# Optimization experiments

Hardware: AMD Instinct MI355X
Metric: run time of the kernel (lower is better)

Reference implementation:

```python
import jax, jax.numpy as jnp
import numpy as np

N = 50000
E = 800000
EPS = 1e-16
NEG_SLOPE = 0.2

def setup_inputs() -> dict:
    key = jax.random.key(0)
    ks = jax.random.split(key, 10)
    s = lambda fan: 1.0 / np.sqrt(fan)
    return {
        "x": jax.random.normal(ks[0], (N, 128), dtype=jnp.float32),
        "edge_index": jax.random.randint(ks[1], (2, E), 0, N, dtype=jnp.int64),
        "W1": jax.random.normal(ks[2], (128, 4 * 32), dtype=jnp.float32) * s(128),
        "att_src1": jax.random.normal(ks[3], (4, 32), dtype=jnp.float32) * s(32),
        "att_dst1": jax.random.normal(ks[4], (4, 32), dtype=jnp.float32) * s(32),
        "b1": jnp.zeros((128,), dtype=jnp.float32),
        "W2": jax.random.normal(ks[5], (128, 2), dtype=jnp.float32) * s(128),
        "att_src2": jax.random.normal(ks[6], (1, 2), dtype=jnp.float32) * s(2),
        "att_dst2": jax.random.normal(ks[7], (1, 2), dtype=jnp.float32) * s(2),
        "b2": jnp.zeros((2,), dtype=jnp.float32),
    }

def _gat_conv(x, src, dst, W, att_src, att_dst, bias, heads, out_ch, concat):
    n = x.shape[0]
    h = (x @ W).reshape(n, heads, out_ch)                      # [N,H,C]
    a_src = jnp.sum(h * att_src[None], axis=-1)                # [N,H]
    a_dst = jnp.sum(h * att_dst[None], axis=-1)                # [N,H]
    e = jax.nn.leaky_relu(a_src[src] + a_dst[dst], NEG_SLOPE)  # [Etot,H]
    # segment softmax over incoming edges per destination node
    m = jax.ops.segment_max(e, dst, num_segments=n)            # [N,H]
    m = jnp.where(jnp.isfinite(m), m, 0.0)
    ex = jnp.exp(e - m[dst])
    denom = jax.ops.segment_sum(ex, dst, num_segments=n)       # [N,H]
    alpha = ex / (denom[dst] + EPS)                            # [Etot,H]
    out = jax.ops.segment_sum(alpha[:, :, None] * h[src], dst, num_segments=n)  # [N,H,C]
    if concat:
        out = out.reshape(n, heads * out_ch)
    else:
        out = out.mean(axis=1)
    return out + bias

def reference(x, edge_index, W1, att_src1, att_dst1, b1, W2, att_src2, att_dst2, b2):
    n = x.shape[0]
    # PyG GATConv adds self-loops by default
    loops = jnp.arange(n, dtype=edge_index.dtype)
    src = jnp.concatenate([edge_index[0], loops])
    dst = jnp.concatenate([edge_index[1], loops])
    # dropout is identity at inference
    h = jax.nn.elu(_gat_conv(x, src, dst, W1, att_src1, att_dst1, b1, 4, 32, True))
    h = _gat_conv(h, src, dst, W2, att_src2, att_dst2, b2, 1, 2, False)
    return jax.nn.log_softmax(h, axis=1)
```

## Files before the change

kernel.cpp:

```cpp
#include <hip/hip_runtime.h>
#include <hip/hip_bf16.h>

#define NN 50000
#define EE 800000
#define CAP 64
#define CSTRIDE 16
#define NEG_SLOPE 0.2f
#define EPSF 1e-16f
#define BUILD_BLOCKS 4096
#define GEMM_BLOCKS ((NN + 63) / 64)
#define NPAIRS (EE / 2)
#define WROW 136
#define PROBE_IDX (NN * CSTRIDE)

typedef unsigned int uint32;
typedef __attribute__((ext_vector_type(8))) short short8;
typedef __attribute__((ext_vector_type(4))) float floatx4;

__device__ __forceinline__ unsigned short f2bf(float f) {
  unsigned int u = __float_as_uint(f);
  unsigned int r = (u + 0x7fffu + ((u >> 16) & 1u)) >> 16;
  return (unsigned short)r;
}
__device__ __forceinline__ float bf_lo(uint32 v) { return __uint_as_float(v << 16); }
__device__ __forceinline__ float bf_hi(uint32 v) { return __uint_as_float(v & 0xffff0000u); }
__device__ __forceinline__ float lrelu(float e) { return fmaxf(e, NEG_SLOPE * e); }

__device__ __forceinline__ void do_build(int b, const int* __restrict__ ei,
                                         int* __restrict__ counts,
                                         int* __restrict__ csr, uint32 P) {
  const int range = b & 7;
  const int lo = range * (NN / 8);
  const int hi = lo + (NN / 8);
  const int group = b >> 3;
  const int tid0 = group * 256 + threadIdx.x;
  const int stride = (BUILD_BLOCKS >> 3) * 256;

  { int n = lo + tid0; if (n < hi) csr[n * CAP] = n; }

  const int2* __restrict__ dst2 = (const int2*)(ei + EE);
  const int2* __restrict__ src2 = (const int2*)(ei);
  for (int p = tid0; p < NPAIRS; p += stride) {
    int2 d2 = dst2[p];
    int2 s2 = src2[p];
    if (d2.x >= lo && d2.x < hi) {
      uint32 k = (uint32)atomicAdd(&counts[d2.x * CSTRIDE], 1) - P;
      if (k < CAP - 1) csr[d2.x * CAP + k + 1] = s2.x;
    }
    if (d2.y >= lo && d2.y < hi) {
      uint32 k = (uint32)atomicAdd(&counts[d2.y * CSTRIDE], 1) - P;
      if (k < CAP - 1) csr[d2.y * CAP + k + 1] = s2.y;
    }
  }
}

__device__ __forceinline__ void do_gemm_tile(
    int tile, const float* __restrict__ x, const unsigned short* __restrict__ WtL,
    const float* __restrict__ att_src1, const float* __restrict__ att_dst1,
    uint32* __restrict__ h1b, float* __restrict__ as1, float* __restrict__ ad1) {
  const int t    = threadIdx.x;
  const int wave = t >> 6;
  const int lane = t & 63;
  const int quad = lane >> 4;
  const int col  = lane & 15;
  const int nodeBase = tile * 64 + wave * 16;

  floatx4 acc[8];
  #pragma unroll
  for (int i = 0; i < 8; i++) acc[i] = (floatx4){0.f, 0.f, 0.f, 0.f};

  int mread = nodeBase + col; if (mread >= NN) mread = NN - 1;
  const float* __restrict__ xrow = x + (size_t)mread * 128 + quad * 8;
  const unsigned short* __restrict__ bbase = WtL + col * WROW + quad * 8;

  #pragma unroll
  for (int ks = 0; ks < 4; ks++) {
    float4 a0 = *(const float4*)(xrow + ks * 32);
    float4 a1 = *(const float4*)(xrow + ks * 32 + 4);
    union { short8 v; unsigned short u[8]; } af;
    af.u[0] = f2bf(a0.x); af.u[1] = f2bf(a0.y);
    af.u[2] = f2bf(a0.z); af.u[3] = f2bf(a0.w);
    af.u[4] = f2bf(a1.x); af.u[5] = f2bf(a1.y);
    af.u[6] = f2bf(a1.z); af.u[7] = f2bf(a1.w);
    #pragma unroll
    for (int tt = 0; tt < 8; tt++) {
      short8 bf = *(const short8*)(bbase + tt * 16 * WROW + ks * 32);
      acc[tt] = __builtin_amdgcn_mfma_f32_16x16x32_bf16(af.v, bf, acc[tt], 0, 0, 0);
    }
  }

  float asv[8], adv[8];
  #pragma unroll
  for (int tt = 0; tt < 8; tt++) {
    asv[tt] = att_src1[tt * 16 + col];
    adv[tt] = att_dst1[tt * 16 + col];
  }

  #pragma unroll
  for (int r = 0; r < 4; r++) {
    const int gn = nodeBase + quad * 4 + r;
    const bool live = (gn < NN);
    #pragma unroll
    for (int tt = 0; tt < 8; tt++) {
      float v = acc[tt][r];
      float w = __shfl_xor(v, 1, 64);
      if (live && ((col & 1) == 0)) {
        uint32 pk = (uint32)f2bf(v) | ((uint32)f2bf(w) << 16);
        h1b[(size_t)gn * 64 + tt * 8 + (col >> 1)] = pk;
      }
    }
    #pragma unroll
    for (int h = 0; h < 4; h++) {
      float ps = acc[2 * h][r] * asv[2 * h] + acc[2 * h + 1][r] * asv[2 * h + 1];
      float pd = acc[2 * h][r] * adv[2 * h] + acc[2 * h + 1][r] * adv[2 * h + 1];
      #pragma unroll
      for (int off = 1; off < 16; off <<= 1) {
        ps += __shfl_xor(ps, off, 64);
        pd += __shfl_xor(pd, off, 64);
      }
      if (live && col == 0) {
        as1[gn * 4 + h] = ps;
        ad1[gn * 4 + h] = pd;
      }
    }
  }
}

__global__ __launch_bounds__(256) void work_k(
    const int* __restrict__ ei, int* __restrict__ counts, int* __restrict__ csr,
    const float* __restrict__ x, const float* __restrict__ W1,
    const float* __restrict__ att_src1, const float* __restrict__ att_dst1,
    uint32* __restrict__ h1b, float* __restrict__ as1, float* __restrict__ ad1) {
  __shared__ unsigned short WtL[128 * WROW];
  const int b = blockIdx.x;
  if (b < GEMM_BLOCKS) {
    const int c  = threadIdx.x & 127;
    const int kh = (threadIdx.x >> 7) * 4;
    #pragma unroll
    for (int k0 = kh; k0 < 128; k0 += 8) {
      unsigned short w0 = f2bf(W1[(k0 + 0) * 128 + c]);
      unsigned short w1 = f2bf(W1[(k0 + 1) * 128 + c]);
      unsigned short w2 = f2bf(W1[(k0 + 2) * 128 + c]);
      unsigned short w3 = f2bf(W1[(k0 + 3) * 128 + c]);
      uint32 lo = (uint32)w0 | ((uint32)w1 << 16);
      uint32 hi = (uint32)w2 | ((uint32)w3 << 16);
      *(uint2*)&WtL[c * WROW + k0] = make_uint2(lo, hi);
    }
    __syncthreads();
    do_gemm_tile(b, x, WtL, att_src1, att_dst1, h1b, as1, ad1);
  } else {
    const uint32 P =
        (uint32)__builtin_amdgcn_readfirstlane(counts[PROBE_IDX]);
    do_build(b - GEMM_BLOCKS, ei, counts, csr, P);
  }
}

__global__ __launch_bounds__(256) void agg1_k(
    const int* __restrict__ counts, const int* __restrict__ csr,
    const uint32* __restrict__ h1b, const float* __restrict__ as1,
    const float* __restrict__ ad1, const float* __restrict__ b1,
    const float* __restrict__ W2, const float* __restrict__ att_src2,
    const float* __restrict__ att_dst2, float4* __restrict__ rec) {
  const int lane = threadIdx.x & 63;
  const int wv = threadIdx.x >> 6;
  const int hd = lane >> 4;
  const int n = __builtin_amdgcn_readfirstlane(blockIdx.x * 4 + wv);

  const uint32 P = (uint32)__builtin_amdgcn_readfirstlane(counts[PROBE_IDX]);
  int cnt = (int)((uint32)counts[n * CSTRIDE] - P) + 1;
  cnt = __builtin_amdgcn_readfirstlane(cnt < CAP ? cnt : CAP);
  const int* __restrict__ row = csr + n * CAP;
  const float adv = ad1[n * 4 + hd];

  float den = 0.f, accx = 0.f, accy = 0.f;
  int j = 0;
  for (; j + 3 < cnt; j += 4) {
    int s0 = __builtin_amdgcn_readfirstlane(row[j]);
    int s1 = __builtin_amdgcn_readfirstlane(row[j + 1]);
    int s2 = __builtin_amdgcn_readfirstlane(row[j + 2]);
    int s3 = __builtin_amdgcn_readfirstlane(row[j + 3]);
    float e0 = as1[s0 * 4 + hd] + adv;
    float e1 = as1[s1 * 4 + hd] + adv;
    float e2 = as1[s2 * 4 + hd] + adv;
    float e3 = as1[s3 * 4 + hd] + adv;
    uint32 v0 = h1b[s0 * 64 + lane];
    uint32 v1 = h1b[s1 * 64 + lane];
    uint32 v2 = h1b[s2 * 64 + lane];
    uint32 v3 = h1b[s3 * 64 + lane];
    e0 = lrelu(e0); e1 = lrelu(e1); e2 = lrelu(e2); e3 = lrelu(e3);
    float x0 = __expf(e0), x1 = __expf(e1), x2 = __expf(e2), x3 = __expf(e3);
    den += (x0 + x1) + (x2 + x3);
    accx = fmaf(x0, bf_lo(v0), accx);
    accy = fmaf(x0, bf_hi(v0), accy);
    accx = fmaf(x1, bf_lo(v1), accx);
    accy = fmaf(x1, bf_hi(v1), accy);
    accx = fmaf(x2, bf_lo(v2), accx);
    accy = fmaf(x2, bf_hi(v2), accy);
    accx = fmaf(x3, bf_lo(v3), accx);
    accy = fmaf(x3, bf_hi(v3), accy);
  }
  for (; j < cnt; j++) {
    int s = __builtin_amdgcn_readfirstlane(row[j]);
    float e = lrelu(as1[s * 4 + hd] + adv);
    float ex = __expf(e);
    uint32 v = h1b[s * 64 + lane];
    den += ex;
    accx = fmaf(ex, bf_lo(v), accx);
    accy = fmaf(ex, bf_hi(v), accy);
  }

  float inv = 1.f / (den + EPSF);
  float2 bb = ((const float2*)b1)[lane];
  float ox = accx * inv + bb.x;
  float oy = accy * inv + bb.y;
  ox = (ox > 0.f) ? ox : (__expf(ox) - 1.f);
  oy = (oy > 0.f) ? oy : (__expf(oy) - 1.f);

  float4 wq = ((const float4*)W2)[lane];
  float p0 = ox * wq.x + oy * wq.z;
  float p1 = ox * wq.y + oy * wq.w;
  #pragma unroll
  for (int off = 32; off; off >>= 1) {
    p0 += __shfl_xor(p0, off, 64);
    p1 += __shfl_xor(p1, off, 64);
  }
  if (lane == 0) {
    rec[n] = make_float4(p0, p1,
                         p0 * att_src2[0] + p1 * att_src2[1],
                         p0 * att_dst2[0] + p1 * att_dst2[1]);
  }
}

__global__ __launch_bounds__(256) void agg2_k(
    const int* __restrict__ counts, const int* __restrict__ csr,
    const float4* __restrict__ rec, const float* __restrict__ b2,
    float* __restrict__ out) {
  int i = blockIdx.x * 256 + threadIdx.x;
  if (i >= NN * 8) return;
  int n = i >> 3;
  int sub = i & 7;
  const float adv = rec[n].w;
  const uint32 P = (uint32)__builtin_amdgcn_readfirstlane(counts[PROBE_IDX]);
  int cnt = (int)((uint32)counts[n * CSTRIDE] - P) + 1;
  cnt = cnt < CAP ? cnt : CAP;
  const int* __restrict__ row = csr + n * CAP;

  float den = 0.f, a0 = 0.f, a1 = 0.f;
  for (int j = sub; j < cnt; j += 8) {
    int s = row[j];
    float4 rs = rec[s];
    float e = lrelu(rs.z + adv);
    float ex = __expf(e);
    den += ex;
    a0 = fmaf(ex, rs.x, a0);
    a1 = fmaf(ex, rs.y, a1);
  }
  #pragma unroll
  for (int off = 4; off; off >>= 1) {
    den += __shfl_down(den, off, 8);
    a0  += __shfl_down(a0, off, 8);
    a1  += __shfl_down(a1, off, 8);
  }
  if (sub == 0) {
    float inv = 1.f / (den + EPSF);
    float o0 = a0 * inv + b2[0];
    float o1 = a1 * inv + b2[1];
    float mx = fmaxf(o0, o1);
    float lse = mx + __logf(__expf(o0 - mx) + __expf(o1 - mx));
    *(float2*)&out[n * 2] = make_float2(o0 - lse, o1 - lse);
  }
}

extern "C" void kernel_launch(void* const* d_in, const int* in_sizes, int n_in,
                              void* d_out, int out_size, void* d_ws, size_t ws_size,
                              hipStream_t stream) {
  const float* x        = (const float*)d_in[0];
  const int*   ei       = (const int*)d_in[1];
  const float* W1       = (const float*)d_in[2];
  const float* att_src1 = (const float*)d_in[3];
  const float* att_dst1 = (const float*)d_in[4];
  const float* b1       = (const float*)d_in[5];
  const float* W2       = (const float*)d_in[6];
  const float* att_src2 = (const float*)d_in[7];
  const float* att_dst2 = (const float*)d_in[8];
  const float* b2       = (const float*)d_in[9];
  float* out = (float*)d_out;

  char* p = (char*)d_ws;
  auto alloc = [&](size_t bytes) {
    char* r = p;
    p += (bytes + 255) & ~size_t(255);
    return r;
  };
  uint32* h1b  = (uint32*)alloc(sizeof(uint32) * NN * 64);
  float* as1   = (float*)alloc(sizeof(float) * NN * 4);
  float* ad1   = (float*)alloc(sizeof(float) * NN * 4);
  float4* rec  = (float4*)alloc(sizeof(float4) * NN);
  int*   counts = (int*)alloc(sizeof(int) * (NN * CSTRIDE + 16));
  int*   csr   = (int*)alloc(sizeof(int) * NN * CAP);

  work_k<<<GEMM_BLOCKS + BUILD_BLOCKS, 256, 0, stream>>>(
      ei, counts, csr, x, W1, att_src1, att_dst1, h1b, as1, ad1);
  agg1_k<<<NN / 4, 256, 0, stream>>>(counts, csr, h1b, as1, ad1, b1, W2,
                                     att_src2, att_dst2, rec);
  agg2_k<<<(NN * 8 + 255) / 256, 256, 0, stream>>>(counts, csr, rec, b2, out);
}
```

Baseline: 169.3 us.

## Store layer-1 features in fp32 and fold log2e into attention logits

The GEMM epilogue now writes the layer-1 projected features as fp32 instead of packed bf16 pairs, dropping the shuffle and pack step. The gather in agg1 loads float2 per lane instead of one packed word. The attention logits are pre-scaled by log2(e), so the softmax can call the raw v_exp_f32 instruction directly instead of __expf. Doubling the gathered feature bytes in agg1 (6.4M edges of random gathers) raises memory traffic, in exchange for dropping the bf16 conversion and getting a slightly cheaper exp.

New measurement: 191.7 us. +13.2%, slower.

```diff
diff --git a/kernel.cpp b/kernel.cpp
--- a/kernel.cpp
+++ b/kernel.cpp
@@ -7,6 +7,7 @@
 #define CSTRIDE 16
 #define NEG_SLOPE 0.2f
 #define EPSF 1e-16f
+#define LOG2E 1.4426950408889634f
 #define BUILD_BLOCKS 4096
 #define GEMM_BLOCKS ((NN + 63) / 64)
 #define NPAIRS (EE / 2)
@@ -22,9 +23,12 @@
   unsigned int r = (u + 0x7fffu + ((u >> 16) & 1u)) >> 16;
   return (unsigned short)r;
 }
-__device__ __forceinline__ float bf_lo(uint32 v) { return __uint_as_float(v << 16); }
-__device__ __forceinline__ float bf_hi(uint32 v) { return __uint_as_float(v & 0xffff0000u); }
 __device__ __forceinline__ float lrelu(float e) { return fmaxf(e, NEG_SLOPE * e); }
+__device__ __forceinline__ float fexp2(float x) {
+  float r;
+  asm("v_exp_f32 %0, %1" : "=v"(r) : "v"(x));
+  return r;
+}
 
 __device__ __forceinline__ void do_build(int b, const int* __restrict__ ei,
                                          int* __restrict__ counts,
@@ -57,7 +61,7 @@
 __device__ __forceinline__ void do_gemm_tile(
     int tile, const float* __restrict__ x, const unsigned short* __restrict__ WtL,
     const float* __restrict__ att_src1, const float* __restrict__ att_dst1,
-    uint32* __restrict__ h1b, float* __restrict__ as1, float* __restrict__ ad1) {
+    float* __restrict__ h1f, float* __restrict__ as1, float* __restrict__ ad1) {
   const int t    = threadIdx.x;
   const int wave = t >> 6;
   const int lane = t & 63;
@@ -92,8 +96,8 @@
   float asv[8], adv[8];
   #pragma unroll
   for (int tt = 0; tt < 8; tt++) {
-    asv[tt] = att_src1[tt * 16 + col];
-    adv[tt] = att_dst1[tt * 16 + col];
+    asv[tt] = att_src1[tt * 16 + col] * LOG2E;
+    adv[tt] = att_dst1[tt * 16 + col] * LOG2E;
   }
 
   #pragma unroll
@@ -102,12 +106,7 @@
     const bool live = (gn < NN);
     #pragma unroll
     for (int tt = 0; tt < 8; tt++) {
-      float v = acc[tt][r];
-      float w = __shfl_xor(v, 1, 64);
-      if (live && ((col & 1) == 0)) {
-        uint32 pk = (uint32)f2bf(v) | ((uint32)f2bf(w) << 16);
-        h1b[(size_t)gn * 64 + tt * 8 + (col >> 1)] = pk;
-      }
+      if (live) h1f[(size_t)gn * 128 + tt * 16 + col] = acc[tt][r];
     }
     #pragma unroll
     for (int h = 0; h < 4; h++) {
@@ -130,7 +129,7 @@
     const int* __restrict__ ei, int* __restrict__ counts, int* __restrict__ csr,
     const float* __restrict__ x, const float* __restrict__ W1,
     const float* __restrict__ att_src1, const float* __restrict__ att_dst1,
-    uint32* __restrict__ h1b, float* __restrict__ as1, float* __restrict__ ad1) {
+    float* __restrict__ h1f, float* __restrict__ as1, float* __restrict__ ad1) {
   __shared__ unsigned short WtL[128 * WROW];
   const int b = blockIdx.x;
   if (b < GEMM_BLOCKS) {
@@ -147,7 +146,7 @@
       *(uint2*)&WtL[c * WROW + k0] = make_uint2(lo, hi);
     }
     __syncthreads();
-    do_gemm_tile(b, x, WtL, att_src1, att_dst1, h1b, as1, ad1);
+    do_gemm_tile(b, x, WtL, att_src1, att_dst1, h1f, as1, ad1);
   } else {
     const uint32 P =
         (uint32)__builtin_amdgcn_readfirstlane(counts[PROBE_IDX]);
@@ -157,7 +156,7 @@
 
 __global__ __launch_bounds__(256) void agg1_k(
     const int* __restrict__ counts, const int* __restrict__ csr,
-    const uint32* __restrict__ h1b, const float* __restrict__ as1,
+    const float* __restrict__ h1f, const float* __restrict__ as1,
     const float* __restrict__ ad1, const float* __restrict__ b1,
     const float* __restrict__ W2, const float* __restrict__ att_src2,
     const float* __restrict__ att_dst2, float4* __restrict__ rec) {
@@ -171,6 +170,7 @@
   cnt = __builtin_amdgcn_readfirstlane(cnt < CAP ? cnt : CAP);
   const int* __restrict__ row = csr + n * CAP;
   const float adv = ad1[n * 4 + hd];
+  const float2* __restrict__ h1v = (const float2*)h1f;
 
   float den = 0.f, accx = 0.f, accy = 0.f;
   int j = 0;
@@ -183,30 +183,30 @@
     float e1 = as1[s1 * 4 + hd] + adv;
     float e2 = as1[s2 * 4 + hd] + adv;
     float e3 = as1[s3 * 4 + hd] + adv;
-    uint32 v0 = h1b[s0 * 64 + lane];
-    uint32 v1 = h1b[s1 * 64 + lane];
-    uint32 v2 = h1b[s2 * 64 + lane];
-    uint32 v3 = h1b[s3 * 64 + lane];
+    float2 v0 = h1v[(size_t)s0 * 64 + lane];
+    float2 v1 = h1v[(size_t)s1 * 64 + lane];
+    float2 v2 = h1v[(size_t)s2 * 64 + lane];
+    float2 v3 = h1v[(size_t)s3 * 64 + lane];
     e0 = lrelu(e0); e1 = lrelu(e1); e2 = lrelu(e2); e3 = lrelu(e3);
-    float x0 = __expf(e0), x1 = __expf(e1), x2 = __expf(e2), x3 = __expf(e3);
+    float x0 = fexp2(e0), x1 = fexp2(e1), x2 = fexp2(e2), x3 = fexp2(e3);
     den += (x0 + x1) + (x2 + x3);
-    accx = fmaf(x0, bf_lo(v0), accx);
-    accy = fmaf(x0, bf_hi(v0), accy);
-    accx = fmaf(x1, bf_lo(v1), accx);
-    accy = fmaf(x1, bf_hi(v1), accy);
-    accx = fmaf(x2, bf_lo(v2), accx);
-    accy = fmaf(x2, bf_hi(v2), accy);
-    accx = fmaf(x3, bf_lo(v3), accx);
-    accy = fmaf(x3, bf_hi(v3), accy);
+    accx = fmaf(x0, v0.x, accx);
+    accy = fmaf(x0, v0.y, accy);
+    accx = fmaf(x1, v1.x, accx);
+    accy = fmaf(x1, v1.y, accy);
+    accx = fmaf(x2, v2.x, accx);
+    accy = fmaf(x2, v2.y, accy);
+    accx = fmaf(x3, v3.x, accx);
+    accy = fmaf(x3, v3.y, accy);
   }
   for (; j < cnt; j++) {
     int s = __builtin_amdgcn_readfirstlane(row[j]);
     float e = lrelu(as1[s * 4 + hd] + adv);
-    float ex = __expf(e);
-    uint32 v = h1b[s * 64 + lane];
+    float ex = fexp2(e);
+    float2 v = h1v[(size_t)s * 64 + lane];
     den += ex;
-    accx = fmaf(ex, bf_lo(v), accx);
-    accy = fmaf(ex, bf_hi(v), accy);
+    accx = fmaf(ex, v.x, accx);
+    accy = fmaf(ex, v.y, accy);
   }
 
   float inv = 1.f / (den + EPSF);
@@ -226,8 +226,8 @@
   }
   if (lane == 0) {
     rec[n] = make_float4(p0, p1,
-                         p0 * att_src2[0] + p1 * att_src2[1],
-                         p0 * att_dst2[0] + p1 * att_dst2[1]);
+                         (p0 * att_src2[0] + p1 * att_src2[1]) * LOG2E,
+                         (p0 * att_dst2[0] + p1 * att_dst2[1]) * LOG2E);
   }
 }
 
@@ -250,7 +250,7 @@
     int s = row[j];
     float4 rs = rec[s];
     float e = lrelu(rs.z + adv);
-    float ex = __expf(e);
+    float ex = fexp2(e);
     den += ex;
     a0 = fmaf(ex, rs.x, a0);
     a1 = fmaf(ex, rs.y, a1);
@@ -292,7 +292,7 @@
     p += (bytes + 255) & ~size_t(255);
     return r;
   };
-  uint32* h1b  = (uint32*)alloc(sizeof(uint32) * NN * 64);
+  float* h1f   = (float*)alloc(sizeof(float) * NN * 128);
   float* as1   = (float*)alloc(sizeof(float) * NN * 4);
   float* ad1   = (float*)alloc(sizeof(float) * NN * 4);
   float4* rec  = (float4*)alloc(sizeof(float4) * NN);
@@ -300,8 +300,8 @@
   int*   csr   = (int*)alloc(sizeof(int) * NN * CAP);
 
   work_k<<<GEMM_BLOCKS + BUILD_BLOCKS, 256, 0, stream>>>(
-      ei, counts, csr, x, W1, att_src1, att_dst1, h1b, as1, ad1);
-  agg1_k<<<NN / 4, 256, 0, stream>>>(counts, csr, h1b, as1, ad1, b1, W2,
+      ei, counts, csr, x, W1, att_src1, att_dst1, h1f, as1, ad1);
+  agg1_k<<<NN / 4, 256, 0, stream>>>(counts, csr, h1f, as1, ad1, b1, W2,
                                      att_src2, att_dst2, rec);
   agg2_k<<<(NN * 8 + 255) / 256, 256, 0, stream>>>(counts, csr, rec, b2, out);
 }
```
